# Performance work log

Hardware: AMD Instinct MI355X
Metric: run time of the kernel (lower is better)

The kernel has to match this reference:

```python
import jax, jax.numpy as jnp
import numpy as np

B, H, W = 4, 256, 256
TARGET_BETA0 = 5
TARGET_LIFETIME = 0.5
LOSS_SCALE = 100.0


def setup_inputs() -> dict:
    key = jax.random.key(0)
    k1, k2 = jax.random.split(key)
    prob_map = jax.random.uniform(k1, (B, 1, H, W), dtype=jnp.float32)
    roi_mask = (jax.random.uniform(k2, (B, 1, H, W)) < 0.9).astype(jnp.float32)
    return {"prob_map": prob_map, "roi_mask": roi_mask}


def _ph0_topk_loss(f):
    """0-dim persistent homology (V-filtration, 4-connectivity) of f:[H,W],
    then standard top-k MSE(target_lifetime) loss. Equivalent to
    cripser.compute_ph_torch(f, maxdim=0, filtration='V') + _standard_loss.
    Algorithm: Kruskal over grid edges with weight max(f[u],f[v]), elder rule.
    All combinatorics run on stop_gradient values; births/deaths are
    differentiable gathers from f at the paired pixel indices."""
    Hh, Ww = f.shape
    N = Hh * Ww
    fv = f.reshape(-1)
    fvc = jax.lax.stop_gradient(fv)

    idx2d = jnp.arange(N, dtype=jnp.int32).reshape(Hh, Ww)
    r_u = idx2d[:, :-1].reshape(-1)  # right edges
    r_v = r_u + 1
    d_u = idx2d[:-1, :].reshape(-1)  # down edges
    d_v = d_u + Ww
    eu = jnp.concatenate([r_u, d_u])
    ev = jnp.concatenate([r_v, d_v])
    ew = jnp.maximum(fvc[eu], fvc[ev])
    order = jnp.argsort(ew)  # process edges by increasing filtration value
    eu, ev = eu[order], ev[order]

    parent0 = jnp.arange(N, dtype=jnp.int32)

    def step(parent, uv):
        u, v = uv[0], uv[1]

        def find(x):
            return jax.lax.while_loop(lambda y: parent[y] != y, lambda y: parent[y], x)

        ru = find(u)
        rv = find(v)
        merge = ru != rv
        # Invariant: a root is the argmin pixel of its component, so
        # fvc[root] is the component's birth value. Elder rule: the root
        # with smaller birth value survives (ties -> smaller index).
        older_u = (fvc[ru] < fvc[rv]) | ((fvc[ru] == fvc[rv]) & (ru < rv))
        keep = jnp.where(older_u, ru, rv)
        die = jnp.where(older_u, rv, ru)
        b_idx = jnp.where(merge, die, -1)  # birth pixel of the dying comp
        d_pix = jnp.where(fvc[u] >= fvc[v], u, v)  # death = max endpoint
        d_idx = jnp.where(merge, d_pix, -1)
        parent = parent.at[die].set(jnp.where(merge, keep, die))
        parent = parent.at[u].set(jnp.where(merge, keep, ru))  # path compression
        parent = parent.at[v].set(jnp.where(merge, keep, rv))
        return parent, (b_idx, d_idx)

    _, (pb, pd_) = jax.lax.scan(step, parent0, jnp.stack([eu, ev], axis=1))

    valid = pb >= 0
    births = fv[jnp.maximum(pb, 0)]
    deaths = fv[jnp.maximum(pd_, 0)]
    life = jnp.where(valid, deaths - births, 0.0)  # lifetimes >= 0

    # sort descending; invalid slots to the end (keys are stop-gradient)
    key_ = jnp.where(valid, jax.lax.stop_gradient(life), -jnp.inf)
    top = jnp.argsort(-key_)[:TARGET_BETA0]
    topk = life[top]
    vk = valid[top]
    n_use = jnp.sum(vk)  # = min(num_finite, target_beta0)
    sq = jnp.where(vk, (topk - TARGET_LIFETIME) ** 2, 0.0)
    return jnp.sum(sq) / jnp.maximum(n_use, 1).astype(f.dtype)


def reference(prob_map, roi_mask):
    prob = prob_map[:, 0] * roi_mask[:, 0]  # roi masking; (1-roi)*0 is a no-op
    filtration = 1.0 - prob
    losses = jax.vmap(_ph0_topk_loss)(filtration)
    return jnp.mean(losses) * LOSS_SCALE
```

## Files before the change

### kernel.cpp

```cpp
#include <hip/hip_runtime.h>
#include <stdint.h>

#define NPIX 65536
#define NRE  65280
#define NE   130560
#define NIMG 4
#define TPB  1024
#define NBLK_L (NIMG*32)
#define TPIX 2048
#define EPAD 4096
#define KMAX 8192
#define HSZ  1024
#define LHSZ 2048
typedef unsigned long long u64;

__device__ __forceinline__ int ufind(unsigned* lbl, int x){
  int r = x, c = (int)lbl[r];
  while (c != r){ r = c; c = (int)lbl[r]; }
  while ((int)lbl[x] != r){ int n = (int)lbl[x]; lbl[x] = (unsigned)r; x = n; }
  return r;
}
__device__ __forceinline__ int ufind16(unsigned short* uf, int x){
  int r = x, c = (int)uf[r];
  while (c != r){ r = c; c = (int)uf[r]; }
  while ((int)uf[x] != r){ int n = (int)uf[x]; uf[x] = (unsigned short)r; x = n; }
  return r;
}

__global__ __launch_bounds__(TPB)
void ph0_local(const float* __restrict__ prob, const float* __restrict__ roi,
               float* __restrict__ Fg, float* __restrict__ LIFEg,
               unsigned* __restrict__ LBLg, u64* __restrict__ LAg,
               unsigned* __restrict__ C, unsigned* __restrict__ C2,
               unsigned* __restrict__ MAPg, unsigned* __restrict__ KGg)
{
  const int blk = blockIdx.x;
  const int img = blk >> 5;
  const int tile = blk & 31;
  const int tr = tile >> 2, tc = tile & 3;
  const int gr0 = tr*32, gc0 = tc*64;
  const int tid = threadIdx.x;
  const int lane = tid & 63;

  const float* pm = prob + img*NPIX;
  const float* rm = roi  + img*NPIX;
  float* F = Fg + img*NPIX;
  float* LIFE = LIFEg + img*NPIX;
  unsigned* LBL = LBLg + img*NPIX;
  unsigned* MAP = MAPg + img*NPIX;
  unsigned* KG  = KGg  + img*NPIX;
  u64* LA = LAg + (size_t)img*NE;

  __shared__ float          sf[TPIX];
  __shared__ unsigned       slbl[TPIX];
  __shared__ unsigned       sme[TPIX];
  __shared__ unsigned short el[2][EPAD];
  __shared__ unsigned       aux[EPAD];
  __shared__ unsigned       bkw[192];
  __shared__ unsigned short bkp[192];
  __shared__ int s_n, s_f;

  for (int p = tid; p < TPIX; p += TPB){
    int gp = ((gr0 + (p>>6))<<8) + gc0 + (p&63);
    float fv = 1.0f - pm[gp]*rm[gp];
    sf[p] = fv; slbl[p] = (unsigned)p;
    F[gp] = fv; LIFE[gp] = 0.0f;
  }
  for (int s = tid; s < 192; s += TPB){
    unsigned wv = 0xFFFFFFFFu; int p = 0; int gq = -1;
    if (s < 32){ if (tc > 0){ p = s*64;        gq = ((gr0+s)<<8)    + gc0 - 1;  } }
    else if (s < 64){ int k=s-32;  if (tc < 3){ p = k*64+63;  gq = ((gr0+k)<<8)  + gc0 + 64; } }
    else if (s < 128){ int k=s-64; if (tr > 0){ p = k;        gq = ((gr0-1)<<8)  + gc0 + k;  } }
    else { int k=s-128;            if (tr < 7){ p = 31*64+k;  gq = ((gr0+32)<<8) + gc0 + k;  } }
    if (gq >= 0){
      int gp = ((gr0 + (p>>6))<<8) + gc0 + (p&63);
      float fp = 1.0f - pm[gp]*rm[gp];
      float fq = 1.0f - pm[gq]*rm[gq];
      wv = __float_as_uint(fmaxf(fp, fq));
    }
    bkw[s] = wv; bkp[s] = (unsigned short)p;
  }
  __syncthreads();

  int M = EPAD, cur = 0; bool first = true;
  for (;;){
    for (int i = tid; i < TPIX; i += TPB) sme[i] = 0xFFFFFFFFu;
    if (tid == 0){ s_n = 0; s_f = 0; }
    __syncthreads();
    if (tid < 192){
      unsigned wv = bkw[tid];
      if (wv != 0xFFFFFFFFu) atomicMin(&sme[ufind(slbl, (int)bkp[tid])], wv);
    }
    int nxt = cur ^ 1;
    int Mpad = (M + 63) & ~63;
    for (int idx = tid; idx < Mpad; idx += TPB){
      bool keep = false; int e=0,u=0,v=0,a=0,b=0;
      if (idx < M){
        e = first ? idx : (int)el[cur][idx];
        bool valid;
        if (e < 2048){ u=e; v=e+1; valid = ((e&63)!=63); }
        else { u=e-2048; v=u+64; valid = ((u>>6)!=31); }
        if (valid){
          a = ufind(slbl,u); b = ufind(slbl,v);
          if (a != b){
            unsigned wb = __float_as_uint(fmaxf(sf[u],sf[v]));
            atomicMin(&sme[a],wb); atomicMin(&sme[b],wb);
            keep = true;
          }
        }
      }
      u64 m = __ballot(keep);
      if (m){
        int pos0 = __popcll(m & ((1ULL<<lane)-1));
        int leader = __ffsll((long long)m)-1;
        int base = 0;
        if (lane == leader) base = atomicAdd(&s_n, __popcll(m));
        base = __shfl(base, leader);
        if (keep){
          el[nxt][base+pos0] = (unsigned short)e;
          aux[base+pos0] = (unsigned)a | ((unsigned)b<<16);
        }
      }
    }
    __syncthreads();
    int n = s_n;
    for (int idx = tid; idx < n; idx += TPB){
      int e = (int)el[nxt][idx];
      unsigned ab = aux[idx];
      int a = (int)(ab & 0xFFFFu), b = (int)(ab >> 16);
      int u, v;
      if (e < 2048){ u = e; v = e + 1; } else { u = e - 2048; v = u + 64; }
      float w = fmaxf(sf[u], sf[v]);
      unsigned wb = __float_as_uint(w);
      float fa = sf[a], fb = sf[b];
      bool bd = (fb < fa) || ((fb == fa) && (b < a));
      int die = bd ? a : b, keep = bd ? b : a;
      if (sme[die] == wb){
        slbl[die] = (unsigned)keep;
        int gd = ((gr0 + (die>>6))<<8) + gc0 + (die&63);
        LIFE[gd] = w - (bd ? fa : fb);
        s_f = 1;
      }
    }
    __syncthreads();
    int fires = s_f;
    M = n; cur = nxt; first = false;
    __syncthreads();
    if (fires == 0 || M == 0) break;
  }

  for (int p = tid; p < TPIX; p += TPB){
    int r = ufind(slbl, p);
    int gp = ((gr0 + (p>>6))<<8) + gc0 + (p&63);
    LBL[gp] = (unsigned)(((gr0 + (r>>6))<<8) + gc0 + (r&63));
  }
  __syncthreads();
  for (int p = tid; p < TPIX; p += TPB){
    if ((int)slbl[p] == p){
      unsigned pos = atomicAdd(&C2[img], 1u);
      sme[p] = pos;
      unsigned gp = (unsigned)(((gr0 + (p>>6))<<8) + gc0 + (p&63));
      MAP[gp] = pos;
      KG[pos] = gp;
    }
  }
  __syncthreads();

  unsigned* hk = (unsigned*)&el[cur ^ 1][0];
  unsigned* hw = slbl;
  for (int i = tid; i < LHSZ; i += TPB){ hk[i] = 0xFFFFFFFFu; hw[i] = 0xFFFFFFFFu; }
  __syncthreads();

  unsigned* ctr = &C[img];
  int Mpad2 = (M + 63) & ~63;
  for (int idx = tid; idx < Mpad2; idx += TPB){
    bool spill = false;
    u64 rec = 0;
    if (idx < M){
      int e = (int)el[cur][idx];
      unsigned ab = aux[idx];
      int a = (int)(ab & 0xFFFFu), b = (int)(ab >> 16);
      int u, v;
      if (e < 2048){ u = e; v = e + 1; } else { u = e - 2048; v = u + 64; }
      unsigned wb = __float_as_uint(fmaxf(sf[u], sf[v]));
      int lo = a < b ? a : b, hi = a < b ? b : a;
      unsigned key = ((unsigned)lo << 11) | (unsigned)hi;
      unsigned h = ((key * 2654435761u) >> 21) & (LHSZ-1);
      bool ins = false;
      #pragma unroll
      for (int t = 0; t < 8; ++t){
        unsigned old = atomicCAS(&hk[h], 0xFFFFFFFFu, key);
        if (old == 0xFFFFFFFFu || old == key){ atomicMin(&hw[h], wb); ins = true; break; }
        h = (h + 1) & (LHSZ-1);
      }
      if (!ins){
        spill = true;
        rec = ((u64)wb << 32) | ((u64)sme[a] << 16) | sme[b];
      }
    }
    u64 m = __ballot(spill);
    if (m){
      int pos0 = __popcll(m & ((1ULL<<lane)-1));
      int leader = __ffsll((long long)m)-1;
      unsigned base = 0;
      if (lane == leader) base = atomicAdd(ctr, (unsigned)__popcll(m));
      base = (unsigned)__shfl((int)base, leader);
      if (spill) LA[base + pos0] = rec;
    }
  }
  __syncthreads();
  for (int h = tid; h < LHSZ; h += TPB){
    unsigned key = hk[h];
    bool ok = (key != 0xFFFFFFFFu);
    u64 rec = 0;
    if (ok){
      int a = (int)(key >> 11), b = (int)(key & 0x7FFu);
      rec = ((u64)hw[h] << 32) | ((u64)sme[a] << 16) | sme[b];
    }
    u64 m = __ballot(ok);
    if (m){
      int pos0 = __popcll(m & ((1ULL<<lane)-1));
      int leader = __ffsll((long long)m)-1;
      unsigned base = 0;
      if (lane == leader) base = atomicAdd(ctr, (unsigned)__popcll(m));
      base = (unsigned)__shfl((int)base, leader);
      if (ok) LA[base + pos0] = rec;
    }
  }
}

#define RUN_ROUNDS_GLOBAL(UF, ME, RNK)                                       \
  for (int k = tid; k < K; k += TPB){                                        \
    unsigned g = kg[k];                                                      \
    UF[k] = (unsigned short)k;                                               \
    RNK[k] = ((u64)__float_as_uint(f[g]) << 32) | g;                         \
  }                                                                          \
  __syncthreads();                                                           \
  for (int rd = 0; rd < 70000 && n > 0; ++rd){                               \
    for (int k = tid; k < K; k += TPB) ME[k] = 0xFFFFFFFFu;                  \
    if (tid == 0) s_n = 0;                                                   \
    __syncthreads();                                                         \
    int Mpad = (n + 63) & ~63;                                               \
    for (int idx = tid; idx < Mpad; idx += TPB){                             \
      bool keep = false; unsigned wb = 0; int a = 0, b = 0;                  \
      if (idx < n){                                                          \
        u64 rec = src[idx];                                                  \
        wb = (unsigned)(rec >> 32);                                          \
        a = (int)((rec >> 16) & 0xFFFFu);                                    \
        b = (int)(rec & 0xFFFFu);                                            \
        a = ufind16(UF, a); b = ufind16(UF, b);                              \
        if (a != b){ atomicMin(&ME[a], wb); atomicMin(&ME[b], wb); keep = true; } \
      }                                                                      \
      u64 m = __ballot(keep);                                                \
      if (m){                                                                \
        int pos0 = __popcll(m & ((1ULL<<lane)-1));                           \
        int leader = __ffsll((long long)m)-1;                                \
        int base = 0;                                                        \
        if (lane == leader) base = atomicAdd(&s_n, __popcll(m));             \
        base = __shfl(base, leader);                                         \
        if (keep) dst[base+pos0] = ((u64)wb<<32)|((u64)(unsigned)a<<16)|(unsigned)b; \
      }                                                                      \
    }                                                                        \
    __syncthreads();                                                         \
    int nn = s_n;                                                            \
    for (int idx = tid; idx < nn; idx += TPB){                               \
      u64 rec = dst[idx];                                                    \
      unsigned wb = (unsigned)(rec >> 32);                                   \
      int a = (int)((rec >> 16) & 0xFFFFu);                                  \
      int b = (int)(rec & 0xFFFFu);                                          \
      bool bd = RNK[b] < RNK[a];                                             \
      int die = bd ? a : b, kp = bd ? b : a;                                 \
      if (ME[die] == wb){                                                    \
        UF[die] = (unsigned short)kp;                                        \
        u64 rk = RNK[die];                                                   \
        life[(unsigned)(rk & 0xFFFFFFFFu)] =                                 \
            __uint_as_float(wb) - __uint_as_float((unsigned)(rk >> 32));     \
      }                                                                      \
    }                                                                        \
    __syncthreads();                                                         \
    u64* t = src; src = dst; dst = t; n = nn;                                \
  }

__global__ __launch_bounds__(TPB)
void ph0_endgame(const float* __restrict__ Fg, float* __restrict__ LIFEg,
                 unsigned* __restrict__ LBLg, unsigned* __restrict__ MAPg,
                 unsigned* __restrict__ KGg, u64* __restrict__ LAg,
                 u64* __restrict__ LBg, u64* __restrict__ GRg,
                 const unsigned* __restrict__ C, const unsigned* __restrict__ C2,
                 float* __restrict__ LOSS, unsigned* __restrict__ DONE,
                 float* __restrict__ out)
{
  const int img = blockIdx.x, tid = threadIdx.x;
  const int lane = tid & 63;
  const float* f = Fg + img*NPIX;
  float* life = LIFEg + img*NPIX;
  unsigned* lblg = LBLg + img*NPIX;
  unsigned* map  = MAPg + img*NPIX;
  const unsigned* kg = KGg + img*NPIX;
  u64* src = LAg + (size_t)img*NE;
  u64* dst = LBg + (size_t)img*NE;
  u64* rnk = GRg + (size_t)img*NPIX;

  __shared__ u64 smem8[7168];
  unsigned short* s_uf = (unsigned short*)smem8;
  unsigned* s_me = (unsigned*)((char*)smem8 + 16384);
  unsigned* s_hk = (unsigned*)((char*)smem8 + 49152);
  unsigned* s_hw = (unsigned*)((char*)smem8 + 53248);
  __shared__ int s_n;

  const int K = (int)C2[img];
  const int nInt = (int)C[img];

  for (int s = tid; s < 2560; s += TPB){
    int gu, gv;
    if (s < 768){ int ci = s >> 8, row = s & 255, col = 63 + (ci<<6); gu = (row<<8)+col; gv = gu+1; }
    else { int k = s - 768; int ri = k >> 8, colh = k & 255, gr = 31 + (ri<<5); gu = (gr<<8)+colh; gv = gu+256; }
    unsigned ia = map[lblg[gu]];
    unsigned ib = map[lblg[gv]];
    unsigned wb = __float_as_uint(fmaxf(f[gu], f[gv]));
    src[nInt + s] = ((u64)wb << 32) | ((u64)ia << 16) | ib;
  }
  int n = nInt + 2560;
  __syncthreads();

  if (K <= KMAX){
    for (int k = tid; k < K; k += TPB){
      unsigned g = kg[k];
      s_uf[k] = (unsigned short)k;
      rnk[k] = ((u64)__float_as_uint(f[g]) << 32) | g;
    }
    __syncthreads();
    for (int rd = 0; rd < 70000 && n > 0; ++rd){
      for (int k = tid; k < K; k += TPB) s_me[k] = 0xFFFFFFFFu;
      s_hk[tid] = 0xFFFFFFFFu; s_hw[tid] = 0xFFFFFFFFu;
      if (tid == 0) s_n = 0;
      __syncthreads();
      int Mpad = (n + 63) & ~63;
      for (int idx = tid; idx < Mpad; idx += TPB){
        bool spill = false; unsigned wb = 0; int a = 0, b = 0;
        if (idx < n){
          u64 rec = src[idx];
          a = (int)((rec >> 16) & 0xFFFFu);
          b = (int)(rec & 0xFFFFu);
          a = ufind16(s_uf, a); b = ufind16(s_uf, b);
          if (a != b){
            wb = (unsigned)(rec >> 32);
            int lo = a < b ? a : b, hi = a < b ? b : a;
            unsigned key = ((unsigned)lo << 13) | (unsigned)hi;
            unsigned h = ((key * 2654435761u) >> 22) & (HSZ-1);
            bool ins = false;
            #pragma unroll
            for (int t = 0; t < 8; ++t){
              unsigned old = atomicCAS(&s_hk[h], 0xFFFFFFFFu, key);
              if (old == 0xFFFFFFFFu || old == key){ atomicMin(&s_hw[h], wb); ins = true; break; }
              h = (h + 1) & (HSZ-1);
            }
            if (!ins){ atomicMin(&s_me[a], wb); atomicMin(&s_me[b], wb); spill = true; }
          }
        }
        u64 m = __ballot(spill);
        if (m){
          int pos0 = __popcll(m & ((1ULL<<lane)-1));
          int leader = __ffsll((long long)m)-1;
          int base = 0;
          if (lane == leader) base = atomicAdd(&s_n, __popcll(m));
          base = __shfl(base, leader);
          if (spill) dst[base+pos0] = ((u64)wb<<32)|((u64)(unsigned)a<<16)|(unsigned)b;
        }
      }
      __syncthreads();
      {
        unsigned key = s_hk[tid];
        bool okk = (key != 0xFFFFFFFFu);
        unsigned wb = 0; int a = 0, b = 0;
        if (okk){
          a = (int)(key >> 13); b = (int)(key & 0x1FFFu);
          wb = s_hw[tid];
          atomicMin(&s_me[a], wb); atomicMin(&s_me[b], wb);
        }
        u64 m = __ballot(okk);
        if (m){
          int pos0 = __popcll(m & ((1ULL<<lane)-1));
          int leader = __ffsll((long long)m)-1;
          int base = 0;
          if (lane == leader) base = atomicAdd(&s_n, __popcll(m));
          base = __shfl(base, leader);
          if (okk) dst[base+pos0] = ((u64)wb<<32)|((u64)(unsigned)a<<16)|(unsigned)b;
        }
      }
      __syncthreads();
      int nn = s_n;
      for (int idx = tid; idx < nn; idx += TPB){
        u64 rec = dst[idx];
        unsigned wb = (unsigned)(rec >> 32);
        int a = (int)((rec >> 16) & 0xFFFFu);
        int b = (int)(rec & 0xFFFFu);
        u64 ra = rnk[a], rb = rnk[b];
        bool bd = rb < ra;
        int die = bd ? a : b, kp = bd ? b : a;
        if (s_me[die] == wb){
          s_uf[die] = (unsigned short)kp;
          u64 rk = bd ? ra : rb;
          life[(unsigned)(rk & 0xFFFFFFFFu)] =
              __uint_as_float(wb) - __uint_as_float((unsigned)(rk >> 32));
        }
      }
      __syncthreads();
      u64* t = src; src = dst; dst = t;
      n = nn;
    }
  } else {
    unsigned short* g_uf = (unsigned short*)lblg;
    unsigned*       g_me = map;
    u64*            g_rnk = rnk;
    RUN_ROUNDS_GLOBAL(g_uf, g_me, g_rnk)
  }

  float* cand = (float*)smem8;
  float* sval = (float*)smem8 + TPB*5;
  int*   sidx = (int*)((float*)smem8 + TPB*6);
  __syncthreads();

  float t5[5] = {-1.f,-1.f,-1.f,-1.f,-1.f};
  for (int i = tid; i < NPIX; i += TPB){
    float v = life[i];
    if (v > t5[4]){
      int j = 4;
      while (j > 0 && t5[j-1] < v){ t5[j] = t5[j-1]; --j; }
      t5[j] = v;
    }
  }
  #pragma unroll
  for (int k = 0; k < 5; ++k) cand[tid*5+k] = t5[k];
  __syncthreads();

  float lsum = 0.0f;
  for (int k = 0; k < 5; ++k){
    float bv = -1.0f; int bi = 0;
    #pragma unroll
    for (int j = 0; j < 5; ++j){
      float v = cand[tid*5+j];
      if (v > bv){ bv = v; bi = tid*5+j; }
    }
    sval[tid] = bv; sidx[tid] = bi;
    __syncthreads();
    for (int off = TPB>>1; off > 0; off >>= 1){
      if (tid < off && sval[tid+off] > sval[tid]){
        sval[tid] = sval[tid+off]; sidx[tid] = sidx[tid+off];
      }
      __syncthreads();
    }
    float win = sval[0];
    if (tid == 0) cand[sidx[0]] = -2.0f;
    float d = win - 0.5f;
    lsum += d*d;
    __syncthreads();
  }

  if (tid == 0){
    atomicExch(&LOSS[img], lsum * 0.2f);
    __threadfence();
    unsigned prev = atomicAdd(DONE, 1u);
    if (prev == NIMG - 1){
      float s = 0.0f;
      #pragma unroll
      for (int i = 0; i < NIMG; ++i) s += atomicAdd(&LOSS[i], 0.0f);
      out[0] = s * 25.0f;
    }
  }
}

extern "C" void kernel_launch(void* const* d_in, const int* in_sizes, int n_in,
                              void* d_out, int out_size, void* d_ws, size_t ws_size,
                              hipStream_t stream)
{
  const float* prob = (const float*)d_in[0];
  const float* roi  = (const float*)d_in[1];
  char* ws = (char*)d_ws;
  const size_t SZL = (size_t)4*NE*8;
  float*    F    = (float*)(ws);
  float*    LIFE = (float*)(ws + (1u<<20));
  unsigned* LBL  = (unsigned*)(ws + (2u<<20));
  unsigned* MAP  = (unsigned*)(ws + (3u<<20));
  unsigned* KG   = (unsigned*)(ws + (4u<<20));
  u64*      LA   = (u64*)(ws + (5u<<20));
  u64*      LB   = (u64*)(ws + (5u<<20) + SZL);
  u64*      GR   = (u64*)(ws + (5u<<20) + 2*SZL);
  unsigned* C    = (unsigned*)(ws + (5u<<20) + 2*SZL + (2u<<20));
  unsigned* C2   = C + 4;
  unsigned* DONE = C + 8;
  float*    LOSS = (float*)((char*)C + 64);
  float*    out  = (float*)d_out;

  hipMemsetAsync(C, 0, 64, stream);
  ph0_local<<<NBLK_L, TPB, 0, stream>>>(prob, roi, F, LIFE, LBL, LA, C, C2, MAP, KG);
  ph0_endgame<<<NIMG, TPB, 0, stream>>>(F, LIFE, LBL, MAP, KG, LA, LB, GR, C, C2, LOSS, DONE, out);
}
```

Measured before the change: 316.5 us.

## Shrink blocks to 256 threads and cut per-round barriers in Boruvka loops

Both kernels drop from 1024 to 256 threads per block. The per-round counters become a triple-buffered shared array, so the extra barrier and the fire flag go away, and the loop stops when the surviving edge count no longer shrinks. In the endgame, the dedup hash table is skipped once few edges remain, so small rounds avoid the hash clear and scan. The aim is lower barrier cost in the latency-bound serial rounds, at the price of fewer threads for the large early rounds.

```diff
diff --git a/kernel.cpp b/kernel.cpp
--- a/kernel.cpp
+++ b/kernel.cpp
@@ -5,7 +5,8 @@
 #define NRE  65280
 #define NE   130560
 #define NIMG 4
-#define TPB  1024
+#define LTPB 256
+#define ETPB 256
 #define NBLK_L (NIMG*32)
 #define TPIX 2048
 #define EPAD 4096
@@ -27,7 +28,7 @@
   return r;
 }
 
-__global__ __launch_bounds__(TPB)
+__global__ __launch_bounds__(LTPB)
 void ph0_local(const float* __restrict__ prob, const float* __restrict__ roi,
                float* __restrict__ Fg, float* __restrict__ LIFEg,
                unsigned* __restrict__ LBLg, u64* __restrict__ LAg,
@@ -58,15 +59,16 @@
   __shared__ unsigned       aux[EPAD];
   __shared__ unsigned       bkw[192];
   __shared__ unsigned short bkp[192];
-  __shared__ int s_n, s_f;
-
-  for (int p = tid; p < TPIX; p += TPB){
+  __shared__ int s_n[3];
+
+  for (int p = tid; p < TPIX; p += LTPB){
     int gp = ((gr0 + (p>>6))<<8) + gc0 + (p&63);
     float fv = 1.0f - pm[gp]*rm[gp];
     sf[p] = fv; slbl[p] = (unsigned)p;
     F[gp] = fv; LIFE[gp] = 0.0f;
   }
-  for (int s = tid; s < 192; s += TPB){
+  if (tid < 3) s_n[tid] = 0;
+  for (int s = tid; s < 192; s += LTPB){
     unsigned wv = 0xFFFFFFFFu; int p = 0; int gq = -1;
     if (s < 32){ if (tc > 0){ p = s*64;        gq = ((gr0+s)<<8)    + gc0 - 1;  } }
     else if (s < 64){ int k=s-32;  if (tc < 3){ p = k*64+63;  gq = ((gr0+k)<<8)  + gc0 + 64; } }
@@ -82,21 +84,21 @@
   }
   __syncthreads();
 
-  int M = EPAD, cur = 0; bool first = true;
-  for (;;){
-    for (int i = tid; i < TPIX; i += TPB) sme[i] = 0xFFFFFFFFu;
-    if (tid == 0){ s_n = 0; s_f = 0; }
+  int M = EPAD, cur = 0;
+  for (int rd = 0; rd < 100000; ++rd){
+    int nxt = cur ^ 1;
+    for (int i = tid; i < TPIX; i += LTPB) sme[i] = 0xFFFFFFFFu;
+    if (tid == 0) s_n[(rd+1)%3] = 0;
     __syncthreads();
     if (tid < 192){
       unsigned wv = bkw[tid];
       if (wv != 0xFFFFFFFFu) atomicMin(&sme[ufind(slbl, (int)bkp[tid])], wv);
     }
-    int nxt = cur ^ 1;
     int Mpad = (M + 63) & ~63;
-    for (int idx = tid; idx < Mpad; idx += TPB){
+    for (int idx = tid; idx < Mpad; idx += LTPB){
       bool keep = false; int e=0,u=0,v=0,a=0,b=0;
       if (idx < M){
-        e = first ? idx : (int)el[cur][idx];
+        e = (rd == 0) ? idx : (int)el[cur][idx];
         bool valid;
         if (e < 2048){ u=e; v=e+1; valid = ((e&63)!=63); }
         else { u=e-2048; v=u+64; valid = ((u>>6)!=31); }
@@ -114,7 +116,7 @@
         int pos0 = __popcll(m & ((1ULL<<lane)-1));
         int leader = __ffsll((long long)m)-1;
         int base = 0;
-        if (lane == leader) base = atomicAdd(&s_n, __popcll(m));
+        if (lane == leader) base = atomicAdd(&s_n[rd%3], __popcll(m));
         base = __shfl(base, leader);
         if (keep){
           el[nxt][base+pos0] = (unsigned short)e;
@@ -123,9 +125,12 @@
       }
     }
     __syncthreads();
-    int n = s_n;
-    for (int idx = tid; idx < n; idx += TPB){
-      int e = (int)el[nxt][idx];
+    int n = s_n[rd%3];
+    cur = nxt;
+    if (n == M || n == 0){ M = n; break; }
+    M = n;
+    for (int idx = tid; idx < M; idx += LTPB){
+      int e = (int)el[cur][idx];
       unsigned ab = aux[idx];
       int a = (int)(ab & 0xFFFFu), b = (int)(ab >> 16);
       int u, v;
@@ -139,23 +144,18 @@
         slbl[die] = (unsigned)keep;
         int gd = ((gr0 + (die>>6))<<8) + gc0 + (die&63);
         LIFE[gd] = w - (bd ? fa : fb);
-        s_f = 1;
       }
     }
     __syncthreads();
-    int fires = s_f;
-    M = n; cur = nxt; first = false;
-    __syncthreads();
-    if (fires == 0 || M == 0) break;
-  }
-
-  for (int p = tid; p < TPIX; p += TPB){
+  }
+
+  for (int p = tid; p < TPIX; p += LTPB){
     int r = ufind(slbl, p);
     int gp = ((gr0 + (p>>6))<<8) + gc0 + (p&63);
     LBL[gp] = (unsigned)(((gr0 + (r>>6))<<8) + gc0 + (r&63));
   }
   __syncthreads();
-  for (int p = tid; p < TPIX; p += TPB){
+  for (int p = tid; p < TPIX; p += LTPB){
     if ((int)slbl[p] == p){
       unsigned pos = atomicAdd(&C2[img], 1u);
       sme[p] = pos;
@@ -168,12 +168,12 @@
 
   unsigned* hk = (unsigned*)&el[cur ^ 1][0];
   unsigned* hw = slbl;
-  for (int i = tid; i < LHSZ; i += TPB){ hk[i] = 0xFFFFFFFFu; hw[i] = 0xFFFFFFFFu; }
+  for (int i = tid; i < LHSZ; i += LTPB){ hk[i] = 0xFFFFFFFFu; hw[i] = 0xFFFFFFFFu; }
   __syncthreads();
 
   unsigned* ctr = &C[img];
   int Mpad2 = (M + 63) & ~63;
-  for (int idx = tid; idx < Mpad2; idx += TPB){
+  for (int idx = tid; idx < Mpad2; idx += LTPB){
     bool spill = false;
     u64 rec = 0;
     if (idx < M){
@@ -209,7 +209,7 @@
     }
   }
   __syncthreads();
-  for (int h = tid; h < LHSZ; h += TPB){
+  for (int h = tid; h < LHSZ; h += LTPB){
     unsigned key = hk[h];
     bool ok = (key != 0xFFFFFFFFu);
     u64 rec = 0;
@@ -230,18 +230,18 @@
 }
 
 #define RUN_ROUNDS_GLOBAL(UF, ME, RNK)                                       \
-  for (int k = tid; k < K; k += TPB){                                        \
+  for (int k = tid; k < K; k += ETPB){                                       \
     unsigned g = kg[k];                                                      \
     UF[k] = (unsigned short)k;                                               \
     RNK[k] = ((u64)__float_as_uint(f[g]) << 32) | g;                         \
   }                                                                          \
   __syncthreads();                                                           \
   for (int rd = 0; rd < 70000 && n > 0; ++rd){                               \
-    for (int k = tid; k < K; k += TPB) ME[k] = 0xFFFFFFFFu;                  \
-    if (tid == 0) s_n = 0;                                                   \
+    for (int k = tid; k < K; k += ETPB) ME[k] = 0xFFFFFFFFu;                 \
+    if (tid == 0) s_n[0] = 0;                                                \
     __syncthreads();                                                         \
     int Mpad = (n + 63) & ~63;                                               \
-    for (int idx = tid; idx < Mpad; idx += TPB){                             \
+    for (int idx = tid; idx < Mpad; idx += ETPB){                            \
       bool keep = false; unsigned wb = 0; int a = 0, b = 0;                  \
       if (idx < n){                                                          \
         u64 rec = src[idx];                                                  \
@@ -256,14 +256,14 @@
         int pos0 = __popcll(m & ((1ULL<<lane)-1));                           \
         int leader = __ffsll((long long)m)-1;                                \
         int base = 0;                                                        \
-        if (lane == leader) base = atomicAdd(&s_n, __popcll(m));             \
+        if (lane == leader) base = atomicAdd(&s_n[0], __popcll(m));          \
         base = __shfl(base, leader);                                         \
         if (keep) dst[base+pos0] = ((u64)wb<<32)|((u64)(unsigned)a<<16)|(unsigned)b; \
       }                                                                      \
     }                                                                        \
     __syncthreads();                                                         \
-    int nn = s_n;                                                            \
-    for (int idx = tid; idx < nn; idx += TPB){                               \
+    int nn = s_n[0];                                                         \
+    for (int idx = tid; idx < nn; idx += ETPB){                              \
       u64 rec = dst[idx];                                                    \
       unsigned wb = (unsigned)(rec >> 32);                                   \
       int a = (int)((rec >> 16) & 0xFFFFu);                                  \
@@ -281,7 +281,7 @@
     u64* t = src; src = dst; dst = t; n = nn;                                \
   }
 
-__global__ __launch_bounds__(TPB)
+__global__ __launch_bounds__(ETPB)
 void ph0_endgame(const float* __restrict__ Fg, float* __restrict__ LIFEg,
                  unsigned* __restrict__ LBLg, unsigned* __restrict__ MAPg,
                  unsigned* __restrict__ KGg, u64* __restrict__ LAg,
@@ -306,12 +306,12 @@
   unsigned* s_me = (unsigned*)((char*)smem8 + 16384);
   unsigned* s_hk = (unsigned*)((char*)smem8 + 49152);
   unsigned* s_hw = (unsigned*)((char*)smem8 + 53248);
-  __shared__ int s_n;
+  __shared__ int s_n[3];
 
   const int K = (int)C2[img];
   const int nInt = (int)C[img];
 
-  for (int s = tid; s < 2560; s += TPB){
+  for (int s = tid; s < 2560; s += ETPB){
     int gu, gv;
     if (s < 768){ int ci = s >> 8, row = s & 255, col = 63 + (ci<<6); gu = (row<<8)+col; gv = gu+1; }
     else { int k = s - 768; int ri = k >> 8, colh = k & 255, gr = 31 + (ri<<5); gu = (gr<<8)+colh; gv = gu+256; }
@@ -320,24 +320,27 @@
     unsigned wb = __float_as_uint(fmaxf(f[gu], f[gv]));
     src[nInt + s] = ((u64)wb << 32) | ((u64)ia << 16) | ib;
   }
+  if (tid < 3) s_n[tid] = 0;
   int n = nInt + 2560;
   __syncthreads();
 
   if (K <= KMAX){
-    for (int k = tid; k < K; k += TPB){
+    for (int k = tid; k < K; k += ETPB){
       unsigned g = kg[k];
       s_uf[k] = (unsigned short)k;
       rnk[k] = ((u64)__float_as_uint(f[g]) << 32) | g;
     }
     __syncthreads();
-    for (int rd = 0; rd < 70000 && n > 0; ++rd){
-      for (int k = tid; k < K; k += TPB) s_me[k] = 0xFFFFFFFFu;
-      s_hk[tid] = 0xFFFFFFFFu; s_hw[tid] = 0xFFFFFFFFu;
-      if (tid == 0) s_n = 0;
+    for (int rd = 0; rd < 70000; ++rd){
+      bool useHash = (n > 1024);
+      for (int k = tid; k < K; k += ETPB) s_me[k] = 0xFFFFFFFFu;
+      if (useHash)
+        for (int h = tid; h < HSZ; h += ETPB){ s_hk[h] = 0xFFFFFFFFu; s_hw[h] = 0xFFFFFFFFu; }
+      if (tid == 0) s_n[(rd+1)%3] = 0;
       __syncthreads();
       int Mpad = (n + 63) & ~63;
-      for (int idx = tid; idx < Mpad; idx += TPB){
-        bool spill = false; unsigned wb = 0; int a = 0, b = 0;
+      for (int idx = tid; idx < Mpad; idx += ETPB){
+        bool app = false; unsigned wb = 0; int a = 0, b = 0;
         if (idx < n){
           u64 rec = src[idx];
           a = (int)((rec >> 16) & 0xFFFFu);
@@ -345,52 +348,59 @@
           a = ufind16(s_uf, a); b = ufind16(s_uf, b);
           if (a != b){
             wb = (unsigned)(rec >> 32);
-            int lo = a < b ? a : b, hi = a < b ? b : a;
-            unsigned key = ((unsigned)lo << 13) | (unsigned)hi;
-            unsigned h = ((key * 2654435761u) >> 22) & (HSZ-1);
-            bool ins = false;
-            #pragma unroll
-            for (int t = 0; t < 8; ++t){
-              unsigned old = atomicCAS(&s_hk[h], 0xFFFFFFFFu, key);
-              if (old == 0xFFFFFFFFu || old == key){ atomicMin(&s_hw[h], wb); ins = true; break; }
-              h = (h + 1) & (HSZ-1);
+            if (useHash){
+              int lo = a < b ? a : b, hi = a < b ? b : a;
+              unsigned key = ((unsigned)lo << 13) | (unsigned)hi;
+              unsigned h = ((key * 2654435761u) >> 22) & (HSZ-1);
+              bool ins = false;
+              #pragma unroll
+              for (int t = 0; t < 8; ++t){
+                unsigned old = atomicCAS(&s_hk[h], 0xFFFFFFFFu, key);
+                if (old == 0xFFFFFFFFu || old == key){ atomicMin(&s_hw[h], wb); ins = true; break; }
+                h = (h + 1) & (HSZ-1);
+              }
+              if (!ins){ atomicMin(&s_me[a], wb); atomicMin(&s_me[b], wb); app = true; }
+            } else {
+              atomicMin(&s_me[a], wb); atomicMin(&s_me[b], wb); app = true;
             }
-            if (!ins){ atomicMin(&s_me[a], wb); atomicMin(&s_me[b], wb); spill = true; }
           }
         }
-        u64 m = __ballot(spill);
+        u64 m = __ballot(app);
         if (m){
           int pos0 = __popcll(m & ((1ULL<<lane)-1));
           int leader = __ffsll((long long)m)-1;
           int base = 0;
-          if (lane == leader) base = atomicAdd(&s_n, __popcll(m));
+          if (lane == leader) base = atomicAdd(&s_n[rd%3], __popcll(m));
           base = __shfl(base, leader);
-          if (spill) dst[base+pos0] = ((u64)wb<<32)|((u64)(unsigned)a<<16)|(unsigned)b;
+          if (app) dst[base+pos0] = ((u64)wb<<32)|((u64)(unsigned)a<<16)|(unsigned)b;
         }
       }
       __syncthreads();
-      {
-        unsigned key = s_hk[tid];
-        bool okk = (key != 0xFFFFFFFFu);
-        unsigned wb = 0; int a = 0, b = 0;
-        if (okk){
-          a = (int)(key >> 13); b = (int)(key & 0x1FFFu);
-          wb = s_hw[tid];
-          atomicMin(&s_me[a], wb); atomicMin(&s_me[b], wb);
+      if (useHash){
+        for (int h = tid; h < HSZ; h += ETPB){
+          unsigned key = s_hk[h];
+          bool okk = (key != 0xFFFFFFFFu);
+          unsigned wb = 0; int a = 0, b = 0;
+          if (okk){
+            a = (int)(key >> 13); b = (int)(key & 0x1FFFu);
+            wb = s_hw[h];
+            atomicMin(&s_me[a], wb); atomicMin(&s_me[b], wb);
+          }
+          u64 m = __ballot(okk);
+          if (m){
+            int pos0 = __popcll(m & ((1ULL<<lane)-1));
+            int leader = __ffsll((long long)m)-1;
+            int base = 0;
+            if (lane == leader) base = atomicAdd(&s_n[rd%3], __popcll(m));
+            base = __shfl(base, leader);
+            if (okk) dst[base+pos0] = ((u64)wb<<32)|((u64)(unsigned)a<<16)|(unsigned)b;
+          }
         }
-        u64 m = __ballot(okk);
-        if (m){
-          int pos0 = __popcll(m & ((1ULL<<lane)-1));
-          int leader = __ffsll((long long)m)-1;
-          int base = 0;
-          if (lane == leader) base = atomicAdd(&s_n, __popcll(m));
-          base = __shfl(base, leader);
-          if (okk) dst[base+pos0] = ((u64)wb<<32)|((u64)(unsigned)a<<16)|(unsigned)b;
-        }
-      }
-      __syncthreads();
-      int nn = s_n;
-      for (int idx = tid; idx < nn; idx += TPB){
+        __syncthreads();
+      }
+      int nn = s_n[rd%3];
+      if (nn == 0 || (!useHash && rd > 0 && nn == n)) break;
+      for (int idx = tid; idx < nn; idx += ETPB){
         u64 rec = dst[idx];
         unsigned wb = (unsigned)(rec >> 32);
         int a = (int)((rec >> 16) & 0xFFFFu);
@@ -417,12 +427,12 @@
   }
 
   float* cand = (float*)smem8;
-  float* sval = (float*)smem8 + TPB*5;
-  int*   sidx = (int*)((float*)smem8 + TPB*6);
+  float* sval = (float*)smem8 + ETPB*5;
+  int*   sidx = (int*)((float*)smem8 + ETPB*6);
   __syncthreads();
 
   float t5[5] = {-1.f,-1.f,-1.f,-1.f,-1.f};
-  for (int i = tid; i < NPIX; i += TPB){
+  for (int i = tid; i < NPIX; i += ETPB){
     float v = life[i];
     if (v > t5[4]){
       int j = 4;
@@ -444,7 +454,7 @@
     }
     sval[tid] = bv; sidx[tid] = bi;
     __syncthreads();
-    for (int off = TPB>>1; off > 0; off >>= 1){
+    for (int off = ETPB>>1; off > 0; off >>= 1){
       if (tid < off && sval[tid+off] > sval[tid]){
         sval[tid] = sval[tid+off]; sidx[tid] = sidx[tid+off];
       }
@@ -493,6 +503,6 @@
   float*    out  = (float*)d_out;
 
   hipMemsetAsync(C, 0, 64, stream);
-  ph0_local<<<NBLK_L, TPB, 0, stream>>>(prob, roi, F, LIFE, LBL, LA, C, C2, MAP, KG);
-  ph0_endgame<<<NIMG, TPB, 0, stream>>>(F, LIFE, LBL, MAP, KG, LA, LB, GR, C, C2, LOSS, DONE, out);
+  ph0_local<<<NBLK_L, LTPB, 0, stream>>>(prob, roi, F, LIFE, LBL, LA, C, C2, MAP, KG);
+  ph0_endgame<<<NIMG, ETPB, 0, stream>>>(F, LIFE, LBL, MAP, KG, LA, LB, GR, C, C2, LOSS, DONE, out);
 }
```

Result: slower. 567.3 us (+79.3%).
